# Kernel optimization log

Measured on AMD Instinct MI355X. Metric: run time of the kernel, lower is better.

## Reference

```python
import jax, jax.numpy as jnp
import numpy as np

MAXTIME = 1406073600
MINTIME = 832550400
SPAN = 10000
TIME_EMB = 100
N_GATE = 8
NUM_INTEREST = 4
DIM = 64
SEQ = 256
BATCH = 1024
ALPHA = 0.1
PI = 3.14159  # matches the literal in the source


def _build_time_table():
    # TimeEncoder: interleaved sin/cos positional table over time buckets.
    n = MAXTIME // SPAN + 3
    pos = np.arange(n, dtype=np.float64)[:, None]
    div = np.exp(np.arange(TIME_EMB // 2, dtype=np.float64) * -(np.log(10000.0) / TIME_EMB))[None, :]
    te = np.zeros((n, TIME_EMB), dtype=np.float32)
    te[:, 0::2] = np.sin(pos * div)
    te[:, 1::2] = np.cos(pos * div)
    return jnp.asarray(te)

_TIME_TABLE = _build_time_table()


def _time_encode(t):
    idx = (t / SPAN).astype(jnp.int32)
    return _TIME_TABLE[idx - jnp.min(idx)]


def setup_inputs() -> dict:
    key = jax.random.key(0)
    ks = jax.random.split(key, 11)
    B, S, D, NI, G = BATCH, SEQ, DIM, NUM_INTEREST, N_GATE
    item_his_emb = jax.random.normal(ks[0], (B, S, D), jnp.float32)
    item_eb = jax.random.normal(ks[1], (B, D), jnp.float32)
    # query times near maxtime, history times strictly earlier -> positive deltas
    t_batch = MAXTIME - 1e6 * jax.random.uniform(ks[2], (B,), jnp.float32)
    t_his = MINTIME + (MAXTIME - MINTIME - 1e6) * jax.random.uniform(ks[3], (B, S), jnp.float32)
    mask = (jax.random.uniform(ks[4], (B, S)) > 0.3).astype(jnp.float32)
    W1 = jax.random.normal(ks[5], (3 * TIME_EMB, 100), jnp.float32) / np.sqrt(3 * TIME_EMB)
    b1 = jnp.zeros((100,), jnp.float32)
    W2 = jax.random.normal(ks[6], (100, 1), jnp.float32) * 0.1
    b2 = jnp.zeros((1,), jnp.float32)
    phase = 100000.0 * jax.random.uniform(ks[7], (1, 1, G), jnp.float32)
    tao = 86400.0 * jnp.array([[[1, 2, 7, 14, 30, 60, 365, 730]]], jnp.float32)
    ratio = 0.3 * jax.random.uniform(ks[8], (1, 1, G), jnp.float32)
    gate_emb = jax.random.normal(ks[9], (1, D, G), jnp.float32)
    w_bilinear = jax.random.normal(ks[10], (S, NI * D, D), jnp.float32)
    return {"item_his_emb": item_his_emb, "item_eb": item_eb, "t_batch": t_batch,
            "t_his": t_his, "mask": mask, "W1": W1, "b1": b1, "W2": W2, "b2": b2,
            "phase": phase, "tao": tao, "ratio": ratio, "gate_emb": gate_emb,
            "w_bilinear": w_bilinear, "ta": 2}


def reference(item_his_emb, item_eb, t_batch, t_his, mask, W1, b1, W2, b2,
              phase, tao, ratio, gate_emb, w_bilinear, ta):
    B, S, D = item_his_emb.shape
    NI = NUM_INTEREST
    # --- time factor ---
    t_tiled = jnp.broadcast_to(t_batch[:, None], (B, S))
    time_feature = jnp.concatenate([_time_encode(t_tiled), _time_encode(t_his),
                                    _time_encode(t_tiled - t_his)], axis=2)  # [B,S,300]
    hidden1 = jax.nn.relu(time_feature @ W1 + b1)
    t_factor = jnp.transpose(jax.nn.sigmoid(hidden1 @ W2 + b2), (0, 2, 1))  # [B,1,S]
    # --- circadian gate factor ---
    phi = jnp.mod(t_his[:, :, None] - phase, tao) / tao  # [B,S,G]
    gate = jnp.where(phi < ratio, jnp.maximum(jnp.sin(PI * phi / ratio), 0.0), ALPHA * phi)
    gate_ratio = jax.nn.softmax(jnp.einsum('bsd,dg->bsg', item_his_emb, gate_emb[0]), axis=2) * gate
    g_factor = jnp.sum(gate_ratio, axis=2)[:, None, :]  # [B,1,S]
    reg1 = jnp.linalg.norm(t_factor)
    reg2 = jnp.linalg.norm(ratio) + jnp.linalg.norm(phase) / 100000.0
    # ta == 2 branch
    loss_reg = 0.1 * reg1 + 1.0 * reg2 + 1.0 / reg1 + 0.1 / reg2
    factor = jnp.broadcast_to(t_factor + g_factor, (B, NI, S))
    # --- bilinear_type == 2 projection ---
    item_emb_hat = jnp.einsum('skd,bsd->bsk', w_bilinear, item_his_emb)  # [B,S,NI*D]
    item_emb_hat = item_emb_hat.reshape(B, S, NI, D).transpose(0, 2, 1, 3)  # [B,NI,S,D]
    hat_iter = jax.lax.stop_gradient(item_emb_hat)
    # --- dynamic routing, 3 iterations ---
    cw = jnp.zeros((B, NI, S), item_his_emb.dtype)
    amask = mask[:, None, :]
    cap = None
    for i in range(3):
        sw = jax.nn.softmax(cw, axis=1)           # softmax over interests
        sw = jnp.where(amask == 0, 0.0, sw)
        src = hat_iter if i < 2 else item_emb_hat
        cap = jnp.einsum('bks,bksd->bkd', sw, src)  # [B,NI,D]
        n2 = jnp.sum(cap * cap, axis=-1, keepdims=True)
        cap = (n2 / (1.0 + n2) / jnp.sqrt(n2 + 1e-9)) * cap  # squash
        if i < 2:
            delta = jnp.einsum('bksd,bkd->bks', hat_iter, cap) * factor
            cw = cw + delta
    interest_capsule = cap  # [B,NI,D]
    # --- hard readout ---
    atten = jax.nn.softmax(jnp.einsum('bkd,bd->bk', interest_capsule, item_eb), axis=1)
    readout = interest_capsule[jnp.arange(B), jnp.argmax(atten, axis=1)]  # [B,D]
    return interest_capsule, readout, loss_reg
```

## Files before the change

kernel.cpp:

```cpp
#include <hip/hip_runtime.h>
#include <math.h>
#include <limits.h>

#define BB 1024
#define SS 256
#define DD 64
#define NI 4
#define NG 8
#define TE_N 100
#define PMAX 57420
#define ROWP 100
#define TPB 16

typedef _Float16 half8 __attribute__((ext_vector_type(8)));
typedef _Float16 half4 __attribute__((ext_vector_type(4)));
typedef float f32x4 __attribute__((ext_vector_type(4)));

#define OFF_FTH   ((size_t)0)
#define OFF_FDF   ((size_t)PMAX*ROWP)
#define OFF_GTB   ((size_t)2*PMAX*ROWP)
#define OFF_FAC   (OFF_GTB + (size_t)BB*ROWP)
#define OFF_SCAL  (OFF_FAC + (size_t)BB*SS)
#define OFF_HAT   (OFF_SCAL + 32)

__global__ void k_init(float* ws){
    if (threadIdx.x == 0){
        int* mi = (int*)(ws + OFF_SCAL);
        mi[0] = INT_MAX; mi[1] = INT_MAX; mi[2] = INT_MAX;
        ws[OFF_SCAL + 4] = 0.0f;
    }
}

__global__ void k_min(const float* __restrict__ tb, const float* __restrict__ th, float* ws){
    int gid = blockIdx.x * blockDim.x + threadIdx.x;
    int stride = gridDim.x * blockDim.x;
    int m0 = INT_MAX, m1 = INT_MAX, m2 = INT_MAX;
    for (int i = gid; i < BB*SS; i += stride){
        float t  = th[i];
        float t2 = tb[i >> 8];
        int i1 = (int)(t / 10000.0f);
        int i2 = (int)((t2 - t) / 10000.0f);
        m1 = min(m1, i1);
        m2 = min(m2, i2);
    }
    if (gid < BB) m0 = (int)(tb[gid] / 10000.0f);
    #pragma unroll
    for (int off = 1; off < 64; off <<= 1){
        m0 = min(m0, __shfl_xor(m0, off));
        m1 = min(m1, __shfl_xor(m1, off));
        m2 = min(m2, __shfl_xor(m2, off));
    }
    if ((threadIdx.x & 63) == 0){
        int* mi = (int*)(ws + OFF_SCAL);
        atomicMin(mi + 0, m0);
        atomicMin(mi + 1, m1);
        atomicMin(mi + 2, m2);
    }
}

__global__ void k_tables(const float* __restrict__ W1, float* ws){
    int pbase = blockIdx.x * TPB;
    int t = threadIdx.x;
    __shared__ float te[TPB][TE_N];
    for (int idx = t; idx < TPB*50; idx += 128){
        int pp = idx / 50, h = idx - pp*50;
        double div = exp((double)h * -0.09210340371976184);
        double a = (double)(pbase + pp) * div;
        te[pp][2*h]   = (float)sin(a);
        te[pp][2*h+1] = (float)cos(a);
    }
    __syncthreads();
    if (t < TE_N){
        float a1[TPB], a2[TPB];
        #pragma unroll
        for (int pp = 0; pp < TPB; pp++){ a1[pp] = 0.f; a2[pp] = 0.f; }
        for (int i = 0; i < TE_N; i++){
            float w1v = W1[(100+i)*100 + t];
            float w2v = W1[(200+i)*100 + t];
            #pragma unroll
            for (int pp = 0; pp < TPB; pp++){
                float v = te[pp][i];
                a1[pp] += v * w1v;
                a2[pp] += v * w2v;
            }
        }
        for (int pp = 0; pp < TPB; pp++){
            int p = pbase + pp;
            if (p < PMAX){
                ws[OFF_FTH + (size_t)p*ROWP + t] = a1[pp];
                ws[OFF_FDF + (size_t)p*ROWP + t] = a2[pp];
            }
        }
    }
}

__global__ void k_gtb(const float* __restrict__ tb, const float* __restrict__ W1,
                      const float* __restrict__ b1, float* ws){
    int b = blockIdx.x;
    int t = threadIdx.x;
    const int* mi = (const int*)(ws + OFF_SCAL);
    int p = (int)(tb[b] / 10000.0f) - mi[0];
    __shared__ float te[TE_N];
    if (t < TE_N/2){
        double div = exp((double)t * -0.09210340371976184);
        double a = (double)p * div;
        te[2*t]   = (float)sin(a);
        te[2*t+1] = (float)cos(a);
    }
    __syncthreads();
    if (t < TE_N){
        float a1 = b1[t];
        for (int i = 0; i < TE_N; i++) a1 += te[i] * W1[i*100 + t];
        ws[OFF_GTB + (size_t)b*ROWP + t] = a1;
    }
}

__global__ void __launch_bounds__(256) k_factor(const float* __restrict__ tbatch,
                         const float* __restrict__ th_, const float* __restrict__ W2,
                         const float* __restrict__ b2, float* ws){
    int b  = blockIdx.x >> 1;
    int sh = blockIdx.x & 1;
    int t  = threadIdx.x;
    int lane = t & 63, wv = t >> 6;
    __shared__ float sgtb[TE_N];
    if (t < TE_N) sgtb[t] = ws[OFF_GTB + (size_t)b*ROWP + t];
    __syncthreads();

    bool tail = (lane < 36);
    float w2a = W2[lane];
    float w2b = tail ? W2[64 + lane] : 0.f;
    float ga  = sgtb[lane];
    float gb  = tail ? sgtb[64 + lane] : 0.f;
    float bias = b2[0];

    int sbase = sh*128 + wv*32;
    const int* mi = (const int*)(ws + OFF_SCAL);
    int pth = 0, pdf = 0;
    if (lane < 32){
        float thv = th_[(size_t)b*SS + sbase + lane];
        float tbv = tbatch[b];
        pth = (int)(thv / 10000.0f) - mi[1];
        pdf = (int)((tbv - thv) / 10000.0f) - mi[2];
        pth = min(max(pth, 0), PMAX-1);
        pdf = min(max(pdf, 0), PMAX-1);
    }

    float tfkeep = 0.f;
    float r1acc  = 0.f;
    #pragma unroll 4
    for (int i = 0; i < 32; i++){
        int p1 = __shfl(pth, i);
        int p2 = __shfl(pdf, i);
        const float* r1 = ws + OFF_FTH + (size_t)p1*ROWP;
        const float* r2 = ws + OFF_FDF + (size_t)p2*ROWP;
        float a  = r1[lane];
        float c  = r2[lane];
        float a2 = tail ? r1[64 + lane] : 0.f;
        float c2 = tail ? r2[64 + lane] : 0.f;
        float h = fmaxf(ga + a + c, 0.f) * w2a;
        if (tail) h += fmaxf(gb + a2 + c2, 0.f) * w2b;
        #pragma unroll
        for (int off = 1; off < 64; off <<= 1) h += __shfl_xor(h, off);
        float tf = 1.f / (1.f + expf(-(h + bias)));
        if (lane == i){ tfkeep = tf; r1acc += tf*tf; }
    }
    if (lane < 32) ws[OFF_FAC + (size_t)b*SS + sbase + lane] = tfkeep;
    #pragma unroll
    for (int off = 1; off < 64; off <<= 1) r1acc += __shfl_xor(r1acc, off);
    if (lane == 0) atomicAdd(ws + OFF_SCAL + 4, r1acc);
}

__global__ void __launch_bounds__(256) k_gate(const float* __restrict__ X,
      const float* __restrict__ th_, const float* __restrict__ phase,
      const float* __restrict__ tao, const float* __restrict__ ratio,
      const float* __restrict__ ge, float* ws){
    __shared__ float sge[NG][DD];
    int t = threadIdx.x;
    for (int i = t; i < DD*NG; i += 256) sge[i & 7][i >> 3] = ge[i];
    __syncthreads();
    int gid = blockIdx.x * 256 + t;

    float lg[NG];
    #pragma unroll
    for (int g = 0; g < NG; g++) lg[g] = 0.f;
    const float4* xr = (const float4*)(X + (size_t)gid*DD);
    #pragma unroll 4
    for (int dc = 0; dc < 16; dc++){
        float4 xv = xr[dc];
        #pragma unroll
        for (int g = 0; g < NG; g++){
            lg[g] += xv.x*sge[g][dc*4+0] + xv.y*sge[g][dc*4+1]
                   + xv.z*sge[g][dc*4+2] + xv.w*sge[g][dc*4+3];
        }
    }
    float mx = lg[0];
    #pragma unroll
    for (int g = 1; g < NG; g++) mx = fmaxf(mx, lg[g]);
    float thv = th_[gid];
    float es = 0.f, gf = 0.f;
    #pragma unroll
    for (int g = 0; g < NG; g++){
        float e = expf(lg[g] - mx);
        es += e;
        float phv = fmodf(thv - phase[g], tao[g]) / tao[g];
        float gv = (phv < ratio[g]) ? fmaxf(sinf(3.14159f*phv/ratio[g]), 0.f) : 0.1f*phv;
        gf += e * gv;
    }
    ws[OFF_FAC + gid] += gf / es;
}

__global__ void __launch_bounds__(512, 2)
k_hat(const float* __restrict__ X, const float* __restrict__ Wb,
      float* __restrict__ hat, int b0, int nb){
    int btile = blockIdx.x;
    int s     = blockIdx.y;
    int t     = threadIdx.x;
    int rows = nb - btile*64; if (rows > 64) rows = 64;

    __shared__ _Float16 lds[40960];

    const float* xbase = X + ((size_t)(b0 + btile*64)*SS + s)*DD;
    #pragma unroll
    for (int i = 0; i < 2; i++){
        int q = t + 512*i;
        int r = q >> 4, jf = q & 15;
        float4 v;
        if (r < rows) v = *(const float4*)(xbase + (size_t)r*SS*DD + jf*4);
        else { v.x = 0.f; v.y = 0.f; v.z = 0.f; v.w = 0.f; }
        half4 h, l;
        h.x = (_Float16)v.x; h.y = (_Float16)v.y; h.z = (_Float16)v.z; h.w = (_Float16)v.w;
        l.x = (_Float16)(v.x - (float)h.x); l.y = (_Float16)(v.y - (float)h.y);
        l.z = (_Float16)(v.z - (float)h.z); l.w = (_Float16)(v.w - (float)h.w);
        int bt = r >> 4, rowin = r & 15;
        int j0 = jf*4;
        int kk = j0 >> 5, jb = (j0 & 31) >> 3, e0 = j0 & 7;
        int lane = rowin + 16*jb;
        int base = ((bt*2 + kk)*2)*512 + lane*8 + e0;
        *(half4*)(lds + base)       = h;
        *(half4*)(lds + base + 512) = l;
    }
    const float* wbase = Wb + (size_t)s*16384;
    #pragma unroll
    for (int i = 0; i < 8; i++){
        int q = t + 512*i;
        int kd = q >> 4, jf = q & 15;
        float4 v = *(const float4*)(wbase + kd*64 + jf*4);
        half4 h, l;
        h.x = (_Float16)v.x; h.y = (_Float16)v.y; h.z = (_Float16)v.z; h.w = (_Float16)v.w;
        l.x = (_Float16)(v.x - (float)h.x); l.y = (_Float16)(v.y - (float)h.y);
        l.z = (_Float16)(v.z - (float)h.z); l.w = (_Float16)(v.w - (float)h.w);
        int kdt = kd >> 4, rowin = kd & 15;
        int j0 = jf*4;
        int kk = j0 >> 5, jb = (j0 & 31) >> 3, e0 = j0 & 7;
        int lane = rowin + 16*jb;
        int base = 8192 + ((kdt*2 + kk)*2)*512 + lane*8 + e0;
        *(half4*)(lds + base)       = h;
        *(half4*)(lds + base + 512) = l;
    }
    __syncthreads();

    int w    = t >> 6;
    int lane = t & 63;
    int wbt  = w >> 1;
    int kdh  = w & 1;

    half8 a[2][2];
    #pragma unroll
    for (int kk = 0; kk < 2; kk++)
        #pragma unroll
        for (int hl = 0; hl < 2; hl++)
            a[kk][hl] = *(half8*)(lds + ((wbt*2 + kk)*2 + hl)*512 + lane*8);

    int brow = (lane >> 4) * 4;
    int bcol = lane & 15;

    #pragma unroll
    for (int kdti = 0; kdti < 8; kdti++){
        int kdt = kdh*8 + kdti;
        const _Float16* wb0 = lds + 8192 + ((kdt*2 + 0)*2)*512 + lane*8;
        const _Float16* wb1 = lds + 8192 + ((kdt*2 + 1)*2)*512 + lane*8;
        half8 bh0 = *(half8*)(wb0);
        half8 bl0 = *(half8*)(wb0 + 512);
        half8 bh1 = *(half8*)(wb1);
        half8 bl1 = *(half8*)(wb1 + 512);
        f32x4 acc = {0.f, 0.f, 0.f, 0.f};
        acc = __builtin_amdgcn_mfma_f32_16x16x32_f16(a[0][0], bh0, acc, 0, 0, 0);
        acc = __builtin_amdgcn_mfma_f32_16x16x32_f16(a[0][0], bl0, acc, 0, 0, 0);
        acc = __builtin_amdgcn_mfma_f32_16x16x32_f16(a[0][1], bh0, acc, 0, 0, 0);
        acc = __builtin_amdgcn_mfma_f32_16x16x32_f16(a[1][0], bh1, acc, 0, 0, 0);
        acc = __builtin_amdgcn_mfma_f32_16x16x32_f16(a[1][0], bl1, acc, 0, 0, 0);
        acc = __builtin_amdgcn_mfma_f32_16x16x32_f16(a[1][1], bh1, acc, 0, 0, 0);
        int kd = kdt*16 + bcol;
        #pragma unroll
        for (int r = 0; r < 4; r++){
            int rl = wbt*16 + brow + r;
            if (rl < rows)
                hat[((size_t)(btile*64 + rl)*SS + s)*256 + kd] = acc[r];
        }
    }
}

__global__ void __launch_bounds__(1024) k_route(const float* __restrict__ eb,
                                                const float* __restrict__ mask_,
                                                const float* __restrict__ ws,
                                                const float* __restrict__ hat,
                                                float* __restrict__ out, int b0){
    int bl = blockIdx.x;
    int b = b0 + bl;
    int t = threadIdx.x;
    int lane = t & 63, wv = t >> 6, k = t & 3;
    __shared__ float part[16][4][64];
    __shared__ float capl[4][68];
    __shared__ float logits[4];
    __shared__ int kms;

    float hat_r[64];
    const float4* hsrc = (const float4*)(hat + (size_t)bl*65536 + (size_t)t*64);
    #pragma unroll
    for (int jc = 0; jc < 16; jc++){
        float4 v = hsrc[jc];
        hat_r[4*jc] = v.x; hat_r[4*jc+1] = v.y; hat_r[4*jc+2] = v.z; hat_r[4*jc+3] = v.w;
    }
    int s = t >> 2;
    float fac = ws[OFF_FAC + (size_t)b*SS + s];
    float mk = mask_[b*SS + s];
    float cw = 0.f;
    float capv = 0.f;

    for (int it = 0; it < 3; ++it){
        float m = fmaxf(cw, __shfl_xor(cw, 1)); m = fmaxf(m, __shfl_xor(m, 2));
        float e = expf(cw - m);
        float ssum = e + __shfl_xor(e, 1); ssum += __shfl_xor(ssum, 2);
        float sw = (mk == 0.f) ? 0.f : (e / ssum);

        #pragma unroll
        for (int c = 0; c < 4; c++){
            float tmp[16];
            #pragma unroll
            for (int i = 0; i < 16; i++) tmp[i] = sw * hat_r[c*16 + i];
            #pragma unroll
            for (int msk = 4; msk < 64; msk <<= 1){
                #pragma unroll
                for (int i = 0; i < 16; i++) tmp[i] += __shfl_xor(tmp[i], msk);
            }
            if (lane < 4){
                #pragma unroll
                for (int i = 0; i < 16; i++) part[wv][lane][c*16 + i] = tmp[i];
            }
        }
        __syncthreads();
        if (t < 256){
            int k2 = t >> 6, d = t & 63;
            float cp = 0.f;
            #pragma unroll
            for (int w2 = 0; w2 < 16; w2++) cp += part[w2][k2][d];
            float q = cp * cp;
            #pragma unroll
            for (int msk = 1; msk < 64; msk <<= 1) q += __shfl_xor(q, msk);
            float sc = q / ((1.f + q) * sqrtf(q + 1e-9f));
            capv = sc * cp;
            capl[k2][d] = capv;
        }
        __syncthreads();
        if (it < 2){
            const float4* cp4 = (const float4*)&capl[k][0];
            float dot = 0.f;
            #pragma unroll
            for (int jc = 0; jc < 16; jc++){
                float4 v = cp4[jc];
                dot += hat_r[4*jc]*v.x + hat_r[4*jc+1]*v.y + hat_r[4*jc+2]*v.z + hat_r[4*jc+3]*v.w;
            }
            cw += dot * fac;
        }
        __syncthreads();
    }

    if (t < 256){
        int k2 = t >> 6, d = t & 63;
        out[(size_t)b*256 + t] = capv;
        float qq = capv * eb[b*DD + d];
        #pragma unroll
        for (int msk = 1; msk < 64; msk <<= 1) qq += __shfl_xor(qq, msk);
        if (lane == 0) logits[k2] = qq;
    }
    __syncthreads();
    if (t == 0){
        float best = logits[0]; int km = 0;
        for (int kk = 1; kk < 4; kk++) if (logits[kk] > best){ best = logits[kk]; km = kk; }
        kms = km;
    }
    __syncthreads();
    if (t < 64) out[(size_t)BB*256 + (size_t)b*64 + t] = capl[kms][t];
}

__global__ void k_final(const float* __restrict__ phase, const float* __restrict__ ratio,
                        float* ws, float* __restrict__ out){
    if (threadIdx.x == 0){
        float r2a = 0.f, r2b = 0.f;
        for (int g = 0; g < NG; g++){ r2a += ratio[g]*ratio[g]; r2b += phase[g]*phase[g]; }
        float reg2 = sqrtf(r2a) + sqrtf(r2b) / 100000.0f;
        float reg1 = sqrtf(ws[OFF_SCAL + 4]);
        out[(size_t)BB*256 + (size_t)BB*64] = 0.1f*reg1 + reg2 + 1.0f/reg1 + 0.1f/reg2;
    }
}

extern "C" void kernel_launch(void* const* d_in, const int* in_sizes, int n_in,
                              void* d_out, int out_size, void* d_ws, size_t ws_size,
                              hipStream_t stream){
    const float* Xh = (const float*)d_in[0];
    const float* eb = (const float*)d_in[1];
    const float* tb = (const float*)d_in[2];
    const float* th = (const float*)d_in[3];
    const float* mk = (const float*)d_in[4];
    const float* W1 = (const float*)d_in[5];
    const float* b1 = (const float*)d_in[6];
    const float* W2 = (const float*)d_in[7];
    const float* b2 = (const float*)d_in[8];
    const float* ph = (const float*)d_in[9];
    const float* ta = (const float*)d_in[10];
    const float* ra = (const float*)d_in[11];
    const float* ge = (const float*)d_in[12];
    const float* wb = (const float*)d_in[13];
    float* out = (float*)d_out;
    float* ws  = (float*)d_ws;

    hipLaunchKernelGGL(k_init,   dim3(1),    dim3(64),  0, stream, ws);
    hipLaunchKernelGGL(k_min,    dim3(256),  dim3(256), 0, stream, tb, th, ws);
    hipLaunchKernelGGL(k_tables, dim3((PMAX+TPB-1)/TPB), dim3(128), 0, stream, W1, ws);
    hipLaunchKernelGGL(k_gtb,    dim3(BB),   dim3(128), 0, stream, tb, W1, b1, ws);
    hipLaunchKernelGGL(k_factor, dim3(2*BB), dim3(256), 0, stream, tb, th, W2, b2, ws);
    hipLaunchKernelGGL(k_gate,   dim3(BB),   dim3(256), 0, stream, Xh, th, ph, ta, ra, ge, ws);

    long wfloats  = (long)(ws_size / sizeof(float));
    long hatavail = wfloats - (long)OFF_HAT;
    int CH = (int)(hatavail / 65536);
    if (CH > BB) CH = BB;
    if (CH >= 128) CH &= ~127;
    if (CH < 1)  CH = 1;
    float* hatbuf = ws + OFF_HAT;
    for (int c0 = 0; c0 < BB; c0 += CH){
        int nb = BB - c0; if (nb > CH) nb = CH;
        int nbt = (nb + 63) / 64;
        hipLaunchKernelGGL(k_hat,   dim3(nbt, 256), dim3(512),  0, stream, Xh, wb, hatbuf, c0, nb);
        hipLaunchKernelGGL(k_route, dim3(nb),       dim3(1024), 0, stream, eb, mk, ws, hatbuf, out, c0);
    }
    hipLaunchKernelGGL(k_final, dim3(1), dim3(64), 0, stream, ph, ra, ws, out);
}
```

Before: 553.3 us.

## Restructure routing kernel to 256 threads streaming hat from memory

The routing kernel goes from 1024 threads that each hold 64 hat values in registers and reduce with many cross-lane shuffles to 256 threads, one per sequence position. Each thread computes the softmax over all four interests locally and writes the weights to shared memory. The weighted capsule sum becomes a strided loop over global hat rows with float4 accumulation and a small four-way shared-memory reduction. The dot-product update rereads the hat row from global memory (likely cached) instead of keeping it in registers. This removes the heavy shuffle-reduction cost but reads hat from memory up to three times per routing iteration, and has less parallelism per block.

```diff
diff --git a/kernel.cpp b/kernel.cpp
--- a/kernel.cpp
+++ b/kernel.cpp
@@ -11,6 +11,7 @@
 #define PMAX 57420
 #define ROWP 100
 #define TPB 16
+#define SWP 260
 
 typedef _Float16 half8 __attribute__((ext_vector_type(8)));
 typedef _Float16 half4 __attribute__((ext_vector_type(4)));
@@ -300,89 +301,83 @@
     }
 }
 
-__global__ void __launch_bounds__(1024) k_route(const float* __restrict__ eb,
-                                                const float* __restrict__ mask_,
-                                                const float* __restrict__ ws,
-                                                const float* __restrict__ hat,
-                                                float* __restrict__ out, int b0){
+__global__ void __launch_bounds__(256) k_route(const float* __restrict__ eb,
+                                               const float* __restrict__ mask_,
+                                               const float* __restrict__ ws,
+                                               const float* __restrict__ hat,
+                                               float* __restrict__ out, int b0){
     int bl = blockIdx.x;
     int b = b0 + bl;
     int t = threadIdx.x;
-    int lane = t & 63, wv = t >> 6, k = t & 3;
-    __shared__ float part[16][4][64];
-    __shared__ float capl[4][68];
+    int lane = t & 63;
+    __shared__ float swL[4*SWP];
+    __shared__ float sdata[4*256];
+    __shared__ float capL[256];
     __shared__ float logits[4];
     __shared__ int kms;
 
-    float hat_r[64];
-    const float4* hsrc = (const float4*)(hat + (size_t)bl*65536 + (size_t)t*64);
-    #pragma unroll
-    for (int jc = 0; jc < 16; jc++){
-        float4 v = hsrc[jc];
-        hat_r[4*jc] = v.x; hat_r[4*jc+1] = v.y; hat_r[4*jc+2] = v.z; hat_r[4*jc+3] = v.w;
-    }
-    int s = t >> 2;
+    int s = t;
+    float cw0 = 0.f, cw1 = 0.f, cw2 = 0.f, cw3 = 0.f;
     float fac = ws[OFF_FAC + (size_t)b*SS + s];
-    float mk = mask_[b*SS + s];
-    float cw = 0.f;
+    float mk  = mask_[(size_t)b*SS + s];
+    int phase = t >> 6, q4 = t & 63, kq = q4 >> 4;
+    int kk2 = t >> 6, dd = t & 63;
+    const float4* hb4 = (const float4*)(hat + (size_t)bl*65536);
     float capv = 0.f;
 
     for (int it = 0; it < 3; ++it){
-        float m = fmaxf(cw, __shfl_xor(cw, 1)); m = fmaxf(m, __shfl_xor(m, 2));
-        float e = expf(cw - m);
-        float ssum = e + __shfl_xor(e, 1); ssum += __shfl_xor(ssum, 2);
-        float sw = (mk == 0.f) ? 0.f : (e / ssum);
-
-        #pragma unroll
-        for (int c = 0; c < 4; c++){
-            float tmp[16];
+        float m = fmaxf(fmaxf(cw0, cw1), fmaxf(cw2, cw3));
+        float e0 = expf(cw0-m), e1 = expf(cw1-m), e2 = expf(cw2-m), e3 = expf(cw3-m);
+        float inv = 1.f / (e0+e1+e2+e3);
+        float mm = (mk == 0.f) ? 0.f : inv;
+        swL[0*SWP+s] = e0*mm; swL[1*SWP+s] = e1*mm;
+        swL[2*SWP+s] = e2*mm; swL[3*SWP+s] = e3*mm;
+        __syncthreads();
+
+        float4 acc = {0.f, 0.f, 0.f, 0.f};
+        #pragma unroll 8
+        for (int i = 0; i < 64; i++){
+            int ss = i*4 + phase;
+            float swv = swL[kq*SWP + ss];
+            float4 hv = hb4[ss*64 + q4];
+            acc.x += swv*hv.x; acc.y += swv*hv.y;
+            acc.z += swv*hv.z; acc.w += swv*hv.w;
+        }
+        *(float4*)(sdata + phase*256 + q4*4) = acc;
+        __syncthreads();
+        float cp = sdata[0*256 + t] + sdata[1*256 + t]
+                 + sdata[2*256 + t] + sdata[3*256 + t];
+        float q = cp*cp;
+        #pragma unroll
+        for (int off = 1; off < 64; off <<= 1) q += __shfl_xor(q, off);
+        float sc = q / ((1.f + q) * sqrtf(q + 1e-9f));
+        capv = sc * cp;
+        capL[t] = capv;
+        __syncthreads();
+
+        if (it < 2){
+            const float4* hrow = hb4 + (size_t)s*64;
+            float d0 = 0.f, d1 = 0.f, d2 = 0.f, d3 = 0.f;
             #pragma unroll
-            for (int i = 0; i < 16; i++) tmp[i] = sw * hat_r[c*16 + i];
-            #pragma unroll
-            for (int msk = 4; msk < 64; msk <<= 1){
-                #pragma unroll
-                for (int i = 0; i < 16; i++) tmp[i] += __shfl_xor(tmp[i], msk);
+            for (int j = 0; j < 16; j++){
+                float4 h0 = hrow[j],      c0 = *(const float4*)(capL + j*4);
+                float4 h1 = hrow[16 + j], c1 = *(const float4*)(capL + 64 + j*4);
+                float4 h2 = hrow[32 + j], c2 = *(const float4*)(capL + 128 + j*4);
+                float4 h3 = hrow[48 + j], c3 = *(const float4*)(capL + 192 + j*4);
+                d0 += h0.x*c0.x + h0.y*c0.y + h0.z*c0.z + h0.w*c0.w;
+                d1 += h1.x*c1.x + h1.y*c1.y + h1.z*c1.z + h1.w*c1.w;
+                d2 += h2.x*c2.x + h2.y*c2.y + h2.z*c2.z + h2.w*c2.w;
+                d3 += h3.x*c3.x + h3.y*c3.y + h3.z*c3.z + h3.w*c3.w;
             }
-            if (lane < 4){
-                #pragma unroll
-                for (int i = 0; i < 16; i++) part[wv][lane][c*16 + i] = tmp[i];
-            }
-        }
-        __syncthreads();
-        if (t < 256){
-            int k2 = t >> 6, d = t & 63;
-            float cp = 0.f;
-            #pragma unroll
-            for (int w2 = 0; w2 < 16; w2++) cp += part[w2][k2][d];
-            float q = cp * cp;
-            #pragma unroll
-            for (int msk = 1; msk < 64; msk <<= 1) q += __shfl_xor(q, msk);
-            float sc = q / ((1.f + q) * sqrtf(q + 1e-9f));
-            capv = sc * cp;
-            capl[k2][d] = capv;
-        }
-        __syncthreads();
-        if (it < 2){
-            const float4* cp4 = (const float4*)&capl[k][0];
-            float dot = 0.f;
-            #pragma unroll
-            for (int jc = 0; jc < 16; jc++){
-                float4 v = cp4[jc];
-                dot += hat_r[4*jc]*v.x + hat_r[4*jc+1]*v.y + hat_r[4*jc+2]*v.z + hat_r[4*jc+3]*v.w;
-            }
-            cw += dot * fac;
-        }
-        __syncthreads();
-    }
-
-    if (t < 256){
-        int k2 = t >> 6, d = t & 63;
-        out[(size_t)b*256 + t] = capv;
-        float qq = capv * eb[b*DD + d];
-        #pragma unroll
-        for (int msk = 1; msk < 64; msk <<= 1) qq += __shfl_xor(qq, msk);
-        if (lane == 0) logits[k2] = qq;
-    }
+            cw0 += d0*fac; cw1 += d1*fac; cw2 += d2*fac; cw3 += d3*fac;
+        }
+    }
+
+    out[(size_t)b*256 + t] = capv;
+    float qq = capv * eb[(size_t)b*DD + dd];
+    #pragma unroll
+    for (int off = 1; off < 64; off <<= 1) qq += __shfl_xor(qq, off);
+    if (lane == 0) logits[kk2] = qq;
     __syncthreads();
     if (t == 0){
         float best = logits[0]; int km = 0;
@@ -390,7 +385,7 @@
         kms = km;
     }
     __syncthreads();
-    if (t < 64) out[(size_t)BB*256 + (size_t)b*64 + t] = capl[kms][t];
+    if (t < 64) out[(size_t)BB*256 + (size_t)b*64 + t] = capL[kms*64 + t];
 }
 
 __global__ void k_final(const float* __restrict__ phase, const float* __restrict__ ratio,
@@ -441,8 +436,8 @@
     for (int c0 = 0; c0 < BB; c0 += CH){
         int nb = BB - c0; if (nb > CH) nb = CH;
         int nbt = (nb + 63) / 64;
-        hipLaunchKernelGGL(k_hat,   dim3(nbt, 256), dim3(512),  0, stream, Xh, wb, hatbuf, c0, nb);
-        hipLaunchKernelGGL(k_route, dim3(nb),       dim3(1024), 0, stream, eb, mk, ws, hatbuf, out, c0);
+        hipLaunchKernelGGL(k_hat,   dim3(nbt, 256), dim3(512), 0, stream, Xh, wb, hatbuf, c0, nb);
+        hipLaunchKernelGGL(k_route, dim3(nb),       dim3(256), 0, stream, eb, mk, ws, hatbuf, out, c0);
     }
     hipLaunchKernelGGL(k_final, dim3(1), dim3(64), 0, stream, ph, ra, ws, out);
 }
```

Measured after the change: 681.6 us. 1.23x slower.
